# Performance work log

Hardware: AMD Instinct MI355X
Metric: run time of the kernel (lower is better)

## Reference

```python
import jax, jax.numpy as jnp
import numpy as np
import math

IN_FEATURE = 4096
OUT_FEATURE = 11008

def setup_inputs() -> dict:
    key = jax.random.key(0)
    k1, k2 = jax.random.split(key)
    x = jax.random.normal(k1, (4, 2048, IN_FEATURE), dtype=jnp.float32)
    # int8 weights in [-128, 127]; keep as int8 (stored as int32 spec-wise but cast to int8 here)
    int8_weights = jax.random.randint(k2, (OUT_FEATURE, IN_FEATURE), -128, 128, dtype=jnp.int32).astype(jnp.int8)
    scaler = jnp.float32(1.0 / 128.0 / math.sqrt(IN_FEATURE))
    return {"x": x, "int8_weights": int8_weights, "scaler": scaler}

def reference(x, int8_weights, scaler):
    # Dequantize int8 weights to fp32, then dense matmul: y = x @ W^T
    fp_weights = int8_weights.astype(jnp.float32) * scaler  # [O, I]
    return jnp.einsum('bsi,oi->bso', x, fp_weights)
```

## Files before the change

kernel.cpp:

```cpp
#include <hip/hip_runtime.h>

typedef __attribute__((ext_vector_type(8))) short short8;
typedef __attribute__((ext_vector_type(8))) unsigned short ushort8;
typedef __attribute__((ext_vector_type(4))) float f32x4;
typedef __attribute__((ext_vector_type(4))) float float4v;
typedef __attribute__((ext_vector_type(4))) int int4v;

#define GLB_CAST(p) ((const __attribute__((address_space(1))) void*)(p))
#define LDS_CAST(p) ((__attribute__((address_space(3))) void*)(p))

__device__ __forceinline__ unsigned short f2bf_rne(float f) {
  unsigned u = __builtin_bit_cast(unsigned, f);
  u += 0x7fffu + ((u >> 16) & 1u);
  return (unsigned short)(u >> 16);
}

__device__ __forceinline__ bool w_looks_int32(const int* wi) {
  bool all_small = true;
#pragma unroll
  for (int i = 0; i < 16; ++i) {
    int v = wi[i];
    if (v > 127 || v < -128) all_small = false;
  }
  return all_small;
}


__global__ void pack_w_kernel(const void* __restrict__ w, int4v* __restrict__ wq, long n16) {
  const bool is32 = w_looks_int32((const int*)w);
  if (!is32) return;
  long stride = (long)gridDim.x * blockDim.x;
  for (long i = blockIdx.x * (long)blockDim.x + threadIdx.x; i < n16; i += stride) {
    const int4v* w4 = (const int4v*)w;
    int4v r;
#pragma unroll
    for (int qd = 0; qd < 4; ++qd) {
      int4v raw = w4[i * 4 + qd];
      r[qd] = (raw[0] & 0xff) | ((raw[1] & 0xff) << 8) | ((raw[2] & 0xff) << 16) | (raw[3] << 24);
    }
    wq[i] = r;
  }
}

__global__ __launch_bounds__(256) void rowquant_kernel(const float* __restrict__ x,
                                                       int4v* __restrict__ q,
                                                       float* __restrict__ rowscale, int K) {
  const int row = blockIdx.x;
  const int tid = threadIdx.x;
  const float4v* xr = (const float4v*)(x + (long)row * K);

  float4v v[4];
  float m = 0.f;
#pragma unroll
  for (int i = 0; i < 4; ++i) {
    v[i] = xr[tid * 4 + i];
#pragma unroll
    for (int j = 0; j < 4; ++j) m = fmaxf(m, fabsf(v[i][j]));
  }
#pragma unroll
  for (int off = 32; off >= 1; off >>= 1) m = fmaxf(m, __shfl_xor(m, off));
  __shared__ float wmax[4];
  if ((tid & 63) == 0) wmax[tid >> 6] = m;
  __syncthreads();
  m = fmaxf(fmaxf(wmax[0], wmax[1]), fmaxf(wmax[2], wmax[3]));

  const float k = (m > 0.f) ? 127.f / m : 0.f;
  int4v r;
#pragma unroll
  for (int i = 0; i < 4; ++i) {
    int wv_ = 0;
#pragma unroll
    for (int j = 0; j < 4; ++j) {
      int b = (int)__builtin_rintf(v[i][j] * k);
      wv_ |= (b & 0xff) << (8 * j);
    }
    r[i] = wv_;
  }
  q[((long)row * K >> 4) + tid] = r;
  if (tid == 0) rowscale[row] = m;
}

__global__ __launch_bounds__(512, 2) void gemm256_i8_kernel(
    const signed char* __restrict__ wraw, const signed char* __restrict__ wq,
    const signed char* __restrict__ A, float* __restrict__ C,
    const float* __restrict__ rowscale, const float* __restrict__ scaler,
    int M, int N, int K) {
  __shared__ __align__(16) char lds[131072];

  const signed char* Bw = w_looks_int32((const int*)wraw) ? wq : wraw;

  const int tid  = threadIdx.x;
  const int lane = tid & 63;
  const int wv   = tid >> 6;
  const int wm   = wv >> 2;
  const int wn   = wv & 3;
  const int fr   = lane & 15;
  const int fq   = lane >> 4;

  const int nwg  = gridDim.x;
  const int orig = blockIdx.x;
  const int ntn  = N >> 8;
  const int ntm  = M >> 8;
  int tm, tn;
  if (((nwg & 7) == 0) && ((ntm & 7) == 0)) {
    const int c     = orig & 7;
    const int w     = orig >> 3;
    const int bandh = ntm >> 3;
    tm = c * bandh + (w % bandh);
    tn = w / bandh;
  } else {
    tm = orig / ntn;
    tn = orig - tm * ntn;
  }
  const long rowBase = (long)tm << 8;
  const long colBase = (long)tn << 8;

  const int    srow  = tid >> 3;
  const int    scolb = (((tid & 7) ^ (srow & 7)) << 4);
  const size_t rowb  = (size_t)K;
  const size_t hstep = rowb << 7;
  const size_t r64   = rowb << 6;
  const char*  gA    = (const char*)A + (rowBase + srow) * rowb + scolb;
  const char*  gB    = (const char*)Bw + (colBase + srow) * rowb + scolb;
  const int    dst   = tid << 4;

#define STAGE(gsrc, loff)                                                                              \
  do {                                                                                                 \
    __builtin_amdgcn_global_load_lds(GLB_CAST(gsrc), LDS_CAST(lds + (loff) + dst), 16, 0, 0);          \
    __builtin_amdgcn_global_load_lds(GLB_CAST((gsrc) + r64), LDS_CAST(lds + (loff) + 8192 + dst), 16, 0, 0); \
  } while (0)

  int offA[4][2], offB[2][2];
#pragma unroll
  for (int i = 0; i < 4; ++i) {
    const int lr = i * 32 + wm * 16 + fr;
    const int sw = (lr & 7) << 4;
#pragma unroll
    for (int kk = 0; kk < 2; ++kk) offA[i][kk] = lr * 128 + ((kk * 64 + fq * 16) ^ sw);
  }
#pragma unroll
  for (int j = 0; j < 2; ++j) {
    const int lr = j * 64 + wn * 16 + fr;
    const int sw = (lr & 7) << 4;
#pragma unroll
    for (int kk = 0; kk < 2; ++kk) offB[j][kk] = lr * 128 + ((kk * 64 + fq * 16) ^ sw);
  }

  int4v acc[8][4] = {};
  int4v af[4][2], bf[4][2];
  const int nt = K >> 7;

  STAGE(gA,         0);
  STAGE(gB,         32768);
  STAGE(gA + hstep, 16384);
  STAGE(gB + hstep, 49152);
  asm volatile("s_waitcnt vmcnt(4)" ::: "memory");
  if (nt > 1) {
    STAGE(gA + 128,         65536);
    STAGE(gB + 128,         65536 + 32768);
    STAGE(gA + hstep + 128, 65536 + 16384);
  }
  asm volatile("s_waitcnt vmcnt(6)" ::: "memory");
  __builtin_amdgcn_s_barrier();

#define PH_BAR() __builtin_amdgcn_s_barrier()
#define LGK0()   asm volatile("s_waitcnt lgkmcnt(0)")

#define TILE_BODY(CUR, NXT, TT)                                                                         \
  do {                                                                                                  \
    const int t_ = (TT);                                                                                \
    const size_t kof1_ = (size_t)(t_ + 1) << 7;                                                         \
    const size_t kof2_ = (size_t)(t_ + 2) << 7;                                                         \
                            \
    _Pragma("unroll") for (int i = 0; i < 4; ++i) {                                                     \
      af[i][0] = *(const int4v*)(lds + (CUR) + offA[i][0]);                                             \
      af[i][1] = *(const int4v*)(lds + (CUR) + offA[i][1]);                                             \
    }                                                                                                   \
    _Pragma("unroll") for (int j = 0; j < 2; ++j) {                                                     \
      bf[j][0] = *(const int4v*)(lds + (CUR) + 32768 + offB[j][0]);                                     \
      bf[j][1] = *(const int4v*)(lds + (CUR) + 32768 + offB[j][1]);                                     \
    }                                                                                                   \
    if (t_ + 1 < nt) STAGE(gB + hstep + kof1_, (NXT) + 49152);                                          \
    PH_BAR(); LGK0();                                                                                   \
    __builtin_amdgcn_s_setprio(1);                                                                      \
    _Pragma("unroll") for (int i = 0; i < 4; ++i) {                                                     \
      _Pragma("unroll") for (int j = 0; j < 2; ++j) {                                                   \
        acc[i][j] = __builtin_amdgcn_mfma_i32_16x16x64_i8(af[i][0], bf[j][0], acc[i][j], 0, 0, 0);      \
        acc[i][j] = __builtin_amdgcn_mfma_i32_16x16x64_i8(af[i][1], bf[j][1], acc[i][j], 0, 0, 0);      \
      }                                                                                                 \
    }                                                                                                   \
    __builtin_amdgcn_s_setprio(0);                                                                      \
    PH_BAR();                                                                                           \
                                             \
    _Pragma("unroll") for (int j = 2; j < 4; ++j) {                                                     \
      bf[j][0] = *(const int4v*)(lds + (CUR) + 49152 + offB[j - 2][0]);                                 \
      bf[j][1] = *(const int4v*)(lds + (CUR) + 49152 + offB[j - 2][1]);                                 \
    }                                                                                                   \
    if (t_ + 2 < nt) STAGE(gA + kof2_, (CUR) + 0);                                                      \
    PH_BAR(); LGK0();                                                                                   \
    __builtin_amdgcn_s_setprio(1);                                                                      \
    _Pragma("unroll") for (int i = 0; i < 4; ++i) {                                                     \
      _Pragma("unroll") for (int j = 2; j < 4; ++j) {                                                   \
        acc[i][j] = __builtin_amdgcn_mfma_i32_16x16x64_i8(af[i][0], bf[j][0], acc[i][j], 0, 0, 0);      \
        acc[i][j] = __builtin_amdgcn_mfma_i32_16x16x64_i8(af[i][1], bf[j][1], acc[i][j], 0, 0, 0);      \
      }                                                                                                 \
    }                                                                                                   \
    __builtin_amdgcn_s_setprio(0);                                                                      \
    PH_BAR();                                                                                           \
                                             \
    _Pragma("unroll") for (int i = 0; i < 4; ++i) {                                                     \
      af[i][0] = *(const int4v*)(lds + (CUR) + 16384 + offA[i][0]);                                     \
      af[i][1] = *(const int4v*)(lds + (CUR) + 16384 + offA[i][1]);                                     \
    }                                                                                                   \
    if (t_ + 2 < nt) STAGE(gB + kof2_, (CUR) + 32768);                                                  \
    PH_BAR(); LGK0();                                                                                   \
    __builtin_amdgcn_s_setprio(1);                                                                      \
    _Pragma("unroll") for (int i = 0; i < 4; ++i) {                                                     \
      _Pragma("unroll") for (int j = 2; j < 4; ++j) {                                                   \
        acc[4 + i][j] = __builtin_amdgcn_mfma_i32_16x16x64_i8(af[i][0], bf[j][0], acc[4 + i][j], 0, 0, 0); \
        acc[4 + i][j] = __builtin_amdgcn_mfma_i32_16x16x64_i8(af[i][1], bf[j][1], acc[4 + i][j], 0, 0, 0); \
      }                                                                                                 \
    }                                                                                                   \
    __builtin_amdgcn_s_setprio(0);                                                                      \
    PH_BAR();                                                                                           \
                                 \
    if (t_ + 2 < nt) STAGE(gA + hstep + kof2_, (CUR) + 16384);                                          \
    PH_BAR();                                                                                           \
    __builtin_amdgcn_s_setprio(1);                                                                      \
    _Pragma("unroll") for (int i = 0; i < 4; ++i) {                                                     \
      _Pragma("unroll") for (int j = 0; j < 2; ++j) {                                                   \
        acc[4 + i][j] = __builtin_amdgcn_mfma_i32_16x16x64_i8(af[i][0], bf[j][0], acc[4 + i][j], 0, 0, 0); \
        acc[4 + i][j] = __builtin_amdgcn_mfma_i32_16x16x64_i8(af[i][1], bf[j][1], acc[4 + i][j], 0, 0, 0); \
      }                                                                                                 \
    }                                                                                                   \
    __builtin_amdgcn_s_setprio(0);                                                                      \
    if (t_ + 2 < nt)      { asm volatile("s_waitcnt vmcnt(6)" ::: "memory"); }                          \
    else if (t_ + 1 < nt) { asm volatile("s_waitcnt vmcnt(0)" ::: "memory"); }                          \
    if (t_ + 1 < nt) PH_BAR();                                                                          \
  } while (0)

  for (int t = 0; t < nt; t += 2) {
    TILE_BODY(0,     65536, t);
    TILE_BODY(65536, 0,     t + 1);
  }
#undef TILE_BODY
#undef PH_BAR
#undef LGK0
#undef STAGE

  const float s = (*scaler) * (1.f / 127.f);
#pragma unroll
  for (int mi = 0; mi < 8; ++mi) {
#pragma unroll
    for (int j = 0; j < 4; ++j) {
      const long row = rowBase + mi * 32 + wm * 16 + fq * 4 + j;
      const float sc = rowscale[row] * s;
      float* cp = C + row * (long)N + colBase + wn * 16 + fr;
#pragma unroll
      for (int nj = 0; nj < 4; ++nj) cp[(size_t)nj * 64] = (float)acc[mi][nj][j] * sc;
    }
  }
}


__global__ void cvt_x_kernel(const float* __restrict__ x, ushort8* __restrict__ xh, long n8) {
  long stride = (long)gridDim.x * blockDim.x;
  for (long i = blockIdx.x * (long)blockDim.x + threadIdx.x; i < n8; i += stride) {
    float4v a = reinterpret_cast<const float4v*>(x)[2 * i + 0];
    float4v b = reinterpret_cast<const float4v*>(x)[2 * i + 1];
    ushort8 r;
#pragma unroll
    for (int j = 0; j < 4; ++j) {
      r[j]     = f2bf_rne(a[j]);
      r[4 + j] = f2bf_rne(b[j]);
    }
    xh[i] = r;
  }
}

__global__ void cvt_w_kernel(const void* __restrict__ w, ushort8* __restrict__ wh,
                             const float* __restrict__ sp, long n16) {
  const float s = *sp;
  const bool is32 = w_looks_int32((const int*)w);
  long stride = (long)gridDim.x * blockDim.x;
  for (long i = blockIdx.x * (long)blockDim.x + threadIdx.x; i < n16; i += stride) {
    unsigned short tmp[16];
    if (is32) {
      const int4v* w4 = (const int4v*)w;
#pragma unroll
      for (int q = 0; q < 4; ++q) {
        int4v raw = w4[i * 4 + q];
#pragma unroll
        for (int j = 0; j < 4; ++j) tmp[4 * q + j] = f2bf_rne((float)raw[j] * s);
      }
    } else {
      int4v raw = reinterpret_cast<const int4v*>(w)[i];
#pragma unroll
      for (int q = 0; q < 4; ++q) {
        int v = raw[q];
        tmp[4 * q + 0] = f2bf_rne((float)(int)(signed char)(v & 0xff) * s);
        tmp[4 * q + 1] = f2bf_rne((float)(int)(signed char)((v >> 8) & 0xff) * s);
        tmp[4 * q + 2] = f2bf_rne((float)(int)(signed char)((v >> 16) & 0xff) * s);
        tmp[4 * q + 3] = f2bf_rne((float)(v >> 24) * s);
      }
    }
    ushort8 r0, r1;
#pragma unroll
    for (int j = 0; j < 8; ++j) { r0[j] = tmp[j]; r1[j] = tmp[8 + j]; }
    wh[2 * i + 0] = r0;
    wh[2 * i + 1] = r1;
  }
}

#define BM 128
#define BN 128
#define BK 32
__global__ __launch_bounds__(256) void gemm_bt_kernel(
    const unsigned short* __restrict__ A, const unsigned short* __restrict__ Bw,
    float* __restrict__ C, int M, int N, int K) {
  __shared__ __align__(16) unsigned short As[BM * BK];
  __shared__ __align__(16) unsigned short Bs[BN * BK];
  const int t = threadIdx.x, lane = t & 63, wv = t >> 6, wr = wv >> 1, wc = wv & 1;
  const long rowBase = (long)blockIdx.y * BM, colBase = (long)blockIdx.x * BN;
  const int r0 = t >> 2, cb0 = (t & 3) * 16, r1 = r0 + 64;
  const char* gA0 = (const char*)(A + (rowBase + r0) * (long)K) + cb0;
  const char* gA1 = (const char*)(A + (rowBase + r1) * (long)K) + cb0;
  const char* gB0 = (const char*)(Bw + (colBase + r0) * (long)K) + cb0;
  const char* gB1 = (const char*)(Bw + (colBase + r1) * (long)K) + cb0;
  char* lA0 = (char*)As + wv * 1024; char* lA1 = (char*)As + 4096 + wv * 1024;
  char* lB0 = (char*)Bs + wv * 1024; char* lB1 = (char*)Bs + 4096 + wv * 1024;
  const int fr = lane & 15, kb = (lane >> 4) * 16;
  const char* aBase = (const char*)As + (wr * 64 + fr) * (BK * 2) + kb;
  const char* bBase = (const char*)Bs + (wc * 64 + fr) * (BK * 2) + kb;
  f32x4 acc[4][4] = {};
  for (int k0 = 0; k0 < K; k0 += BK) {
    const long koff = (long)k0 * 2;
    __builtin_amdgcn_global_load_lds(GLB_CAST(gA0 + koff), LDS_CAST(lA0), 16, 0, 0);
    __builtin_amdgcn_global_load_lds(GLB_CAST(gA1 + koff), LDS_CAST(lA1), 16, 0, 0);
    __builtin_amdgcn_global_load_lds(GLB_CAST(gB0 + koff), LDS_CAST(lB0), 16, 0, 0);
    __builtin_amdgcn_global_load_lds(GLB_CAST(gB1 + koff), LDS_CAST(lB1), 16, 0, 0);
    __syncthreads();
    short8 af[4], bfv[4];
#pragma unroll
    for (int mi = 0; mi < 4; ++mi) af[mi] = *reinterpret_cast<const short8*>(aBase + mi * 16 * (BK * 2));
#pragma unroll
    for (int nj = 0; nj < 4; ++nj) bfv[nj] = *reinterpret_cast<const short8*>(bBase + nj * 16 * (BK * 2));
#pragma unroll
    for (int mi = 0; mi < 4; ++mi)
#pragma unroll
      for (int nj = 0; nj < 4; ++nj)
        acc[mi][nj] = __builtin_amdgcn_mfma_f32_16x16x32_bf16(af[mi], bfv[nj], acc[mi][nj], 0, 0, 0);
    __syncthreads();
  }
  const int fq = lane >> 4;
#pragma unroll
  for (int mi = 0; mi < 4; ++mi)
#pragma unroll
    for (int j = 0; j < 4; ++j) {
      const long row = rowBase + wr * 64 + mi * 16 + fq * 4 + j;
      float* cp = C + row * (long)N + colBase + wc * 64 + fr;
#pragma unroll
      for (int nj = 0; nj < 4; ++nj) cp[nj * 16] = acc[mi][nj][j];
    }
}

__global__ void gemm_naive_kernel(const float* __restrict__ x, const void* __restrict__ w,
                                  const float* __restrict__ sp, float* __restrict__ out,
                                  int M, int N, int K) {
  const bool is32 = w_looks_int32((const int*)w);
  int n = blockIdx.x * 16 + threadIdx.x;
  int m = blockIdx.y * 16 + threadIdx.y;
  if (m >= M || n >= N) return;
  const float* xr = x + (long)m * K;
  float acc = 0.f;
  if (is32) {
    const int* wr_ = (const int*)w + (long)n * K;
    for (int k = 0; k < K; ++k) acc += xr[k] * (float)wr_[k];
  } else {
    const signed char* wr_ = (const signed char*)w + (long)n * K;
    for (int k = 0; k < K; ++k) acc += xr[k] * (float)wr_[k];
  }
  out[(long)m * N + n] = acc * (*sp);
}

extern "C" void kernel_launch(void* const* d_in, const int* in_sizes, int n_in,
                              void* d_out, int out_size, void* d_ws, size_t ws_size,
                              hipStream_t stream) {
  const float* x      = (const float*)d_in[0];
  const void*  w      = (const void*)d_in[1];
  const float* scaler = (const float*)d_in[2];
  float*       out    = (float*)d_out;

  const int K = 4096;
  const int N = 11008;
  const int M = in_sizes[0] / K;

  const size_t xq_bytes = (size_t)M * K;
  const size_t wq_bytes = (size_t)N * K;
  const size_t rs_bytes = (size_t)M * 4;
  const size_t i8_need  = xq_bytes + wq_bytes + rs_bytes + 64;

  if ((M % 256 == 0) && (N % 256 == 0) && (K == 4096) && ws_size >= i8_need) {
    signed char* xq = (signed char*)d_ws;
    signed char* wq = (signed char*)((char*)d_ws + xq_bytes);
    float*       rs = (float*)((char*)d_ws + xq_bytes + wq_bytes);

    pack_w_kernel<<<512, 256, 0, stream>>>(w, (int4v*)wq, (long)N * K / 16);
    rowquant_kernel<<<M, 256, 0, stream>>>(x, (int4v*)xq, rs, K);
    gemm256_i8_kernel<<<dim3((M / 256) * (N / 256)), 512, 0, stream>>>(
        (const signed char*)w, wq, xq, out, rs, scaler, M, N, K);
    return;
  }

  const size_t xh_bytes = (size_t)M * K * 2;
  const size_t wh_bytes = (size_t)N * K * 2;
  if (ws_size < xh_bytes + wh_bytes) {
    dim3 g((N + 15) / 16, (M + 15) / 16), b(16, 16);
    gemm_naive_kernel<<<g, b, 0, stream>>>(x, w, scaler, out, M, N, K);
    return;
  }

  unsigned short* xh = (unsigned short*)d_ws;
  unsigned short* wh = (unsigned short*)((char*)d_ws + xh_bytes);
  cvt_x_kernel<<<2048, 256, 0, stream>>>(x, (ushort8*)xh, (long)M * K / 8);
  cvt_w_kernel<<<2048, 256, 0, stream>>>(w, (ushort8*)wh, scaler, (long)N * K / 16);
  gemm_bt_kernel<<<dim3(N / BN, M / BM), 256, 0, stream>>>(xh, wh, out, M, N, K);
}
```

Measured before the change: 476.9 us.

## Double-buffer MFMA fragments and reorder quadrants to overlap LDS reads with MFMA

Splits the A and B fragment registers into separate halves (afA/afB, bf01/bf23) and reorders the four MFMA quadrants so each phase loads the fragments the next phase needs while the current MFMAs run. The explicit lgkmcnt(0) waits are dropped, leaving the compiler to insert waits only where data is consumed. The next tile's first fragments are prefetched at the end of each tile. This costs more VGPRs for fragments. The prefetch reads LDS written by other waves before the barrier, which could race with their direct-to-LDS loads.

```diff
diff --git a/kernel.cpp b/kernel.cpp
--- a/kernel.cpp
+++ b/kernel.cpp
@@ -147,7 +147,7 @@
   }
 
   int4v acc[8][4] = {};
-  int4v af[4][2], bf[4][2];
+  int4v afA[4][2], afB[4][2], bf01[2][2], bf23[2][2];
   const int nt = K >> 7;
 
   STAGE(gA,         0);
@@ -161,82 +161,94 @@
     STAGE(gA + hstep + 128, 65536 + 16384);
   }
   asm volatile("s_waitcnt vmcnt(6)" ::: "memory");
+#pragma unroll
+  for (int i = 0; i < 4; ++i) {
+    afA[i][0] = *(const int4v*)(lds + offA[i][0]);
+    afA[i][1] = *(const int4v*)(lds + offA[i][1]);
+  }
+#pragma unroll
+  for (int j = 0; j < 2; ++j) {
+    bf01[j][0] = *(const int4v*)(lds + 32768 + offB[j][0]);
+    bf01[j][1] = *(const int4v*)(lds + 32768 + offB[j][1]);
+  }
   __builtin_amdgcn_s_barrier();
 
 #define PH_BAR() __builtin_amdgcn_s_barrier()
-#define LGK0()   asm volatile("s_waitcnt lgkmcnt(0)")
 
 #define TILE_BODY(CUR, NXT, TT)                                                                         \
   do {                                                                                                  \
     const int t_ = (TT);                                                                                \
     const size_t kof1_ = (size_t)(t_ + 1) << 7;                                                         \
     const size_t kof2_ = (size_t)(t_ + 2) << 7;                                                         \
-                            \
-    _Pragma("unroll") for (int i = 0; i < 4; ++i) {                                                     \
-      af[i][0] = *(const int4v*)(lds + (CUR) + offA[i][0]);                                             \
-      af[i][1] = *(const int4v*)(lds + (CUR) + offA[i][1]);                                             \
-    }                                                                                                   \
+                                    \
     _Pragma("unroll") for (int j = 0; j < 2; ++j) {                                                     \
-      bf[j][0] = *(const int4v*)(lds + (CUR) + 32768 + offB[j][0]);                                     \
-      bf[j][1] = *(const int4v*)(lds + (CUR) + 32768 + offB[j][1]);                                     \
+      bf23[j][0] = *(const int4v*)(lds + (CUR) + 49152 + offB[j][0]);                                   \
+      bf23[j][1] = *(const int4v*)(lds + (CUR) + 49152 + offB[j][1]);                                   \
     }                                                                                                   \
     if (t_ + 1 < nt) STAGE(gB + hstep + kof1_, (NXT) + 49152);                                          \
-    PH_BAR(); LGK0();                                                                                   \
+    PH_BAR();                                                                                           \
     __builtin_amdgcn_s_setprio(1);                                                                      \
     _Pragma("unroll") for (int i = 0; i < 4; ++i) {                                                     \
       _Pragma("unroll") for (int j = 0; j < 2; ++j) {                                                   \
-        acc[i][j] = __builtin_amdgcn_mfma_i32_16x16x64_i8(af[i][0], bf[j][0], acc[i][j], 0, 0, 0);      \
-        acc[i][j] = __builtin_amdgcn_mfma_i32_16x16x64_i8(af[i][1], bf[j][1], acc[i][j], 0, 0, 0);      \
+        acc[i][j] = __builtin_amdgcn_mfma_i32_16x16x64_i8(afA[i][0], bf01[j][0], acc[i][j], 0, 0, 0);   \
+        acc[i][j] = __builtin_amdgcn_mfma_i32_16x16x64_i8(afA[i][1], bf01[j][1], acc[i][j], 0, 0, 0);   \
       }                                                                                                 \
     }                                                                                                   \
     __builtin_amdgcn_s_setprio(0);                                                                      \
     PH_BAR();                                                                                           \
-                                             \
-    _Pragma("unroll") for (int j = 2; j < 4; ++j) {                                                     \
-      bf[j][0] = *(const int4v*)(lds + (CUR) + 49152 + offB[j - 2][0]);                                 \
-      bf[j][1] = *(const int4v*)(lds + (CUR) + 49152 + offB[j - 2][1]);                                 \
+                                     \
+    _Pragma("unroll") for (int i = 0; i < 4; ++i) {                                                     \
+      afB[i][0] = *(const int4v*)(lds + (CUR) + 16384 + offA[i][0]);                                    \
+      afB[i][1] = *(const int4v*)(lds + (CUR) + 16384 + offA[i][1]);                                    \
     }                                                                                                   \
     if (t_ + 2 < nt) STAGE(gA + kof2_, (CUR) + 0);                                                      \
-    PH_BAR(); LGK0();                                                                                   \
-    __builtin_amdgcn_s_setprio(1);                                                                      \
-    _Pragma("unroll") for (int i = 0; i < 4; ++i) {                                                     \
-      _Pragma("unroll") for (int j = 2; j < 4; ++j) {                                                   \
-        acc[i][j] = __builtin_amdgcn_mfma_i32_16x16x64_i8(af[i][0], bf[j][0], acc[i][j], 0, 0, 0);      \
-        acc[i][j] = __builtin_amdgcn_mfma_i32_16x16x64_i8(af[i][1], bf[j][1], acc[i][j], 0, 0, 0);      \
-      }                                                                                                 \
-    }                                                                                                   \
-    __builtin_amdgcn_s_setprio(0);                                                                      \
-    PH_BAR();                                                                                           \
-                                             \
-    _Pragma("unroll") for (int i = 0; i < 4; ++i) {                                                     \
-      af[i][0] = *(const int4v*)(lds + (CUR) + 16384 + offA[i][0]);                                     \
-      af[i][1] = *(const int4v*)(lds + (CUR) + 16384 + offA[i][1]);                                     \
-    }                                                                                                   \
-    if (t_ + 2 < nt) STAGE(gB + kof2_, (CUR) + 32768);                                                  \
-    PH_BAR(); LGK0();                                                                                   \
-    __builtin_amdgcn_s_setprio(1);                                                                      \
-    _Pragma("unroll") for (int i = 0; i < 4; ++i) {                                                     \
-      _Pragma("unroll") for (int j = 2; j < 4; ++j) {                                                   \
-        acc[4 + i][j] = __builtin_amdgcn_mfma_i32_16x16x64_i8(af[i][0], bf[j][0], acc[4 + i][j], 0, 0, 0); \
-        acc[4 + i][j] = __builtin_amdgcn_mfma_i32_16x16x64_i8(af[i][1], bf[j][1], acc[4 + i][j], 0, 0, 0); \
-      }                                                                                                 \
-    }                                                                                                   \
-    __builtin_amdgcn_s_setprio(0);                                                                      \
-    PH_BAR();                                                                                           \
-                                 \
-    if (t_ + 2 < nt) STAGE(gA + hstep + kof2_, (CUR) + 16384);                                          \
     PH_BAR();                                                                                           \
     __builtin_amdgcn_s_setprio(1);                                                                      \
     _Pragma("unroll") for (int i = 0; i < 4; ++i) {                                                     \
       _Pragma("unroll") for (int j = 0; j < 2; ++j) {                                                   \
-        acc[4 + i][j] = __builtin_amdgcn_mfma_i32_16x16x64_i8(af[i][0], bf[j][0], acc[4 + i][j], 0, 0, 0); \
-        acc[4 + i][j] = __builtin_amdgcn_mfma_i32_16x16x64_i8(af[i][1], bf[j][1], acc[4 + i][j], 0, 0, 0); \
+        acc[i][2 + j] = __builtin_amdgcn_mfma_i32_16x16x64_i8(afA[i][0], bf23[j][0], acc[i][2 + j], 0, 0, 0); \
+        acc[i][2 + j] = __builtin_amdgcn_mfma_i32_16x16x64_i8(afA[i][1], bf23[j][1], acc[i][2 + j], 0, 0, 0); \
+      }                                                                                                 \
+    }                                                                                                   \
+    __builtin_amdgcn_s_setprio(0);                                                                      \
+    PH_BAR();                                                                                           \
+                                                   \
+    if (t_ + 2 < nt) STAGE(gB + kof2_, (CUR) + 32768);                                                  \
+    PH_BAR();                                                                                           \
+    __builtin_amdgcn_s_setprio(1);                                                                      \
+    _Pragma("unroll") for (int i = 0; i < 4; ++i) {                                                     \
+      _Pragma("unroll") for (int j = 0; j < 2; ++j) {                                                   \
+        acc[4 + i][2 + j] = __builtin_amdgcn_mfma_i32_16x16x64_i8(afB[i][0], bf23[j][0], acc[4 + i][2 + j], 0, 0, 0); \
+        acc[4 + i][2 + j] = __builtin_amdgcn_mfma_i32_16x16x64_i8(afB[i][1], bf23[j][1], acc[4 + i][2 + j], 0, 0, 0); \
+      }                                                                                                 \
+    }                                                                                                   \
+    __builtin_amdgcn_s_setprio(0);                                                                      \
+    PH_BAR();                                                                                           \
+                   \
+    if (t_ + 2 < nt) STAGE(gA + hstep + kof2_, (CUR) + 16384);                                          \
+    PH_BAR();                                                                                           \
+    __builtin_amdgcn_s_setprio(1);                                                                      \
+    _Pragma("unroll") for (int i = 0; i < 4; ++i) {                                                     \
+      _Pragma("unroll") for (int j = 0; j < 2; ++j) {                                                   \
+        acc[4 + i][j] = __builtin_amdgcn_mfma_i32_16x16x64_i8(afB[i][0], bf01[j][0], acc[4 + i][j], 0, 0, 0); \
+        acc[4 + i][j] = __builtin_amdgcn_mfma_i32_16x16x64_i8(afB[i][1], bf01[j][1], acc[4 + i][j], 0, 0, 0); \
       }                                                                                                 \
     }                                                                                                   \
     __builtin_amdgcn_s_setprio(0);                                                                      \
     if (t_ + 2 < nt)      { asm volatile("s_waitcnt vmcnt(6)" ::: "memory"); }                          \
     else if (t_ + 1 < nt) { asm volatile("s_waitcnt vmcnt(0)" ::: "memory"); }                          \
-    if (t_ + 1 < nt) PH_BAR();                                                                          \
+    if (t_ + 1 < nt) {                                                                                  \
+                                    \
+      _Pragma("unroll") for (int i = 0; i < 4; ++i) {                                                   \
+        afA[i][0] = *(const int4v*)(lds + (NXT) + offA[i][0]);                                          \
+        afA[i][1] = *(const int4v*)(lds + (NXT) + offA[i][1]);                                          \
+      }                                                                                                 \
+      _Pragma("unroll") for (int j = 0; j < 2; ++j) {                                                   \
+        bf01[j][0] = *(const int4v*)(lds + (NXT) + 32768 + offB[j][0]);                                 \
+        bf01[j][1] = *(const int4v*)(lds + (NXT) + 32768 + offB[j][1]);                                 \
+      }                                                                                                 \
+      PH_BAR();                                                                                         \
+    }                                                                                                   \
   } while (0)
 
   for (int t = 0; t < nt; t += 2) {
@@ -245,7 +257,6 @@
   }
 #undef TILE_BODY
 #undef PH_BAR
-#undef LGK0
 #undef STAGE
 
   const float s = (*scaler) * (1.f / 127.f);
```

After: 525.0 us. +10.1%, slower.
